# Optimization experiments

Hardware: AMD Instinct MI355X
Metric: run time of the kernel (lower is better)

The kernel has to match this reference:

```python
import jax, jax.numpy as jnp
import numpy as np

NEG_INF = -1e30  # stands in for float('-inf'); avoids nan in masked softmax edge cases


def setup_inputs() -> dict:
    key = jax.random.key(0)
    ks = jax.random.split(key, 6)
    B, N, MD, QD, AD = 64, 512, 1024, 1024, 1024
    stdv_m = 1.0 / np.sqrt(MD)
    stdv_q = 1.0 / np.sqrt(QD)
    stdv_a = 1.0 / np.sqrt(AD)
    return {
        "memory_values": jax.random.normal(ks[0], (B, N, MD), dtype=jnp.float32),
        "mask": jax.random.randint(ks[1], (B, N), 0, 2, dtype=jnp.int32),
        "query": jax.random.normal(ks[2], (B, QD), dtype=jnp.float32),
        "Wh": jax.random.uniform(ks[3], (MD, AD), jnp.float32, -stdv_m, stdv_m),
        "Ws": jax.random.uniform(ks[4], (QD, AD), jnp.float32, -stdv_q, stdv_q),
        "v": jax.random.uniform(ks[5], (AD, 1), jnp.float32, -stdv_a, stdv_a),
    }


def reference(memory_values, mask, query, Wh, Ws, v):
    # Et(i) = tanh(Hi*Wh + St*Ws) @ v ; At = softmax(Et) with masking
    tq = query @ Ws                                   # (B, AD)
    h = jnp.tanh(memory_values @ Wh + tq[:, None, :])  # (B, N, AD)
    logits = jnp.squeeze(h @ v, axis=-1)              # (B, N)

    maskf = mask.astype(logits.dtype)
    # no_cells[b] == 1 iff every cell in row b is masked out
    no_cells = jnp.prod(1.0 - maskf, axis=1, keepdims=True)  # (B, 1)
    suppress = jnp.where(maskf == 0, NEG_INF, 0.0)
    suppress = jnp.where(no_cells == 1.0, 0.0, suppress)
    weights = jax.nn.softmax(logits + suppress, axis=-1)
    weights = jnp.where(no_cells == 1.0, 0.0, weights)

    context = jnp.einsum("bn,bnd->bd", weights, memory_values)
    return context
```

## Files before the change

### kernel.cpp

```cpp
#include <hip/hip_runtime.h>
#include <cstdint>
#include <cstddef>

typedef float floatx4 __attribute__((ext_vector_type(4)));
typedef _Float16 half8_t __attribute__((ext_vector_type(8)));
typedef _Float16 half2_t __attribute__((ext_vector_type(2)));

#define AS1 __attribute__((address_space(1)))
#define AS3 __attribute__((address_space(3)))

__device__ __forceinline__ void glds16(const void* g, void* l) {
  __builtin_amdgcn_global_load_lds((const AS1 void*)g, (AS3 void*)l, 16, 0, 0);
}

__device__ __forceinline__ half2_t pkrtz(float a, float b) {
  return __builtin_bit_cast(half2_t, __builtin_amdgcn_cvt_pkrtz(a, b));
}

__device__ __forceinline__ float fast_tanh(float x) {
  float e2 = __expf(2.f * x);
  return 1.f - 2.f * __builtin_amdgcn_rcpf(e2 + 1.f);
}

__global__ __launch_bounds__(256) void k_prep(
    const float* __restrict__ mem, _Float16* __restrict__ memh,
    const float* __restrict__ Wh, _Float16* __restrict__ WhT,
    const float* __restrict__ q, const float* __restrict__ Ws,
    float* __restrict__ tq) {
  __shared__ float sh[64 * 65];
  const int bx = blockIdx.x;
  const int tid = threadIdx.x;
  if (bx >= 1280) {
    size_t i = (((size_t)(bx - 1280) << 8) + tid) << 3;
    floatx4 a = *(const floatx4*)(mem + i);
    floatx4 b = *(const floatx4*)(mem + i + 4);
    union { half2_t h2[4]; half8_t h8; } u;
    u.h2[0] = half2_t{(_Float16)a[0], (_Float16)a[1]};
    u.h2[1] = half2_t{(_Float16)a[2], (_Float16)a[3]};
    u.h2[2] = half2_t{(_Float16)b[0], (_Float16)b[1]};
    u.h2[3] = half2_t{(_Float16)b[2], (_Float16)b[3]};
    *(half8_t*)(memh + i) = u.h8;
  } else if (bx < 256) {
    int bb = bx;
    int n0 = (bb & 15) << 6, k0 = (bb >> 4) << 6;
    int tx = tid & 63, ty = tid >> 6;
    #pragma unroll
    for (int r = ty; r < 64; r += 4) sh[r * 65 + tx] = Wh[(size_t)(k0 + r) * 1024 + n0 + tx];
    __syncthreads();
    #pragma unroll
    for (int r = ty; r < 64; r += 4)
      WhT[(size_t)(n0 + r) * 1024 + k0 + tx] = (_Float16)sh[tx * 65 + r];
  } else {
    int bb = bx - 256;
    int d0 = (bb & 15) << 6, b = bb >> 4;
    int dl = tid & 63, kg = tid >> 6;
    float* qs = sh;
    float* red = sh + 1024;
    for (int k = tid; k < 1024; k += 256) qs[k] = q[(b << 10) + k];
    __syncthreads();
    float acc = 0.f;
    int kbase = kg << 8;
    #pragma unroll 8
    for (int k = 0; k < 256; ++k)
      acc += qs[kbase + k] * Ws[(size_t)(kbase + k) * 1024 + d0 + dl];
    red[(kg << 6) + dl] = acc;
    __syncthreads();
    if (kg == 0)
      tq[(b << 10) + d0 + dl] = red[dl] + red[64 + dl] + red[128 + dl] + red[192 + dl];
  }
}

__global__ void k0_transpose(const float* __restrict__ Wh, _Float16* __restrict__ WhT) {
  __shared__ float t[64][65];
  int k0 = blockIdx.y << 6, n0 = blockIdx.x << 6;
  int tx = threadIdx.x, ty = threadIdx.y;
  #pragma unroll
  for (int r = ty; r < 64; r += 4) t[r][tx] = Wh[(size_t)(k0 + r) * 1024 + n0 + tx];
  __syncthreads();
  #pragma unroll
  for (int r = ty; r < 64; r += 4)
    WhT[(size_t)(n0 + r) * 1024 + k0 + tx] = (_Float16)t[tx][r];
}

__global__ __launch_bounds__(256) void k1_tq(const float* __restrict__ q,
                                             const float* __restrict__ Ws,
                                             float* __restrict__ tq) {
  __shared__ float qs[1024];
  __shared__ float red[4][64];
  int b = blockIdx.y;
  int d0 = blockIdx.x << 6;
  int dl = threadIdx.x & 63, kg = threadIdx.x >> 6;
  for (int k = threadIdx.x; k < 1024; k += 256) qs[k] = q[(b << 10) + k];
  __syncthreads();
  float acc = 0.f;
  int kbase = kg << 8;
  #pragma unroll 8
  for (int k = 0; k < 256; ++k)
    acc += qs[kbase + k] * Ws[(size_t)(kbase + k) * 1024 + d0 + dl];
  red[kg][dl] = acc;
  __syncthreads();
  if (kg == 0)
    tq[(b << 10) + d0 + dl] = red[0][dl] + red[1][dl] + red[2][dl] + red[3][dl];
}

__global__ __launch_bounds__(512, 2) void k2_8ph(
    const _Float16* __restrict__ Ah, const _Float16* __restrict__ BT,
    const float* __restrict__ tq, const float* __restrict__ v,
    float* __restrict__ partials) {
  extern __shared__ char smem[];
  const int bid = blockIdx.x;
  const int wg = ((bid & 7) << 6) | (bid >> 3);
  const int mtile = wg >> 2, ntile = wg & 3;
  const int m0 = mtile << 8, n0 = ntile << 8;
  const int tid = threadIdx.x;
  const int w = tid >> 6, lane = tid & 63;
  const int wm = w >> 2, wn = w & 3, quad = lane >> 4, l15 = lane & 15;

  int aoff[2][4], boff[2][2];
  #pragma unroll
  for (int ks = 0; ks < 2; ++ks) {
    int swz = ((ks << 2) + quad) ^ (l15 & 7);
    #pragma unroll
    for (int i = 0; i < 4; ++i)
      aoff[ks][i] = (wm << 14) + (((i << 4) + l15) << 7) + (swz << 4);
    #pragma unroll
    for (int j = 0; j < 2; ++j)
      boff[ks][j] = 65536 + (wn << 12) + (((j << 4) + l15) << 7) + (swz << 4);
  }

  const int rr = tid >> 3, cc = tid & 7;
  const int r5 = rr & 31;
  int aSrc[2][2], bSrc[2][2], dA[2][2], dB[2][2];
  #pragma unroll
  for (int h = 0; h < 2; ++h)
    #pragma unroll
    for (int hm = 0; hm < 2; ++hm) {
      aSrc[h][hm] = ((m0 + (hm << 7) + (h << 6) + rr) << 10) + ((cc ^ (rr & 7)) << 3);
      dA[h][hm] = (((hm << 1) + h) << 13) + (w << 10);
    }
  #pragma unroll
  for (int ch = 0; ch < 2; ++ch)
    #pragma unroll
    for (int is = 0; is < 2; ++is) {
      int wnb = (is << 1) + (rr >> 5);
      bSrc[ch][is] = ((n0 + (wnb << 6) + (ch << 5) + r5) << 10) + ((cc ^ (r5 & 7)) << 3);
      dB[ch][is] = 65536 + (ch << 14) + (is << 13) + (w << 10);
    }

  floatx4 acc[8][4];
  #pragma unroll
  for (int i = 0; i < 8; ++i)
    #pragma unroll
    for (int j = 0; j < 4; ++j) acc[i][j] = floatx4{0.f, 0.f, 0.f, 0.f};

  half8_t af[2][4], bf[2][2][2];

#define STAGE_A(H, KST, OO)                                   \
  glds16(Ah + aSrc[H][0] + (KST), smem + (OO) + dA[H][0]);    \
  glds16(Ah + aSrc[H][1] + (KST), smem + (OO) + dA[H][1]);
#define STAGE_B(CH, KST, OO)                                  \
  glds16(BT + bSrc[CH][0] + (KST), smem + (OO) + dB[CH][0]);  \
  glds16(BT + bSrc[CH][1] + (KST), smem + (OO) + dB[CH][1]);
#define VMCNT8 asm volatile("s_waitcnt vmcnt(8)" ::: "memory");
#define LOAD_AF(CO, RHOFF)                                    \
  _Pragma("unroll")                                           \
  for (int ks_ = 0; ks_ < 2; ++ks_) {                         \
    _Pragma("unroll")                                         \
    for (int i_ = 0; i_ < 4; ++i_)                            \
      af[ks_][i_] = *(const half8_t*)(smem + (CO) + (RHOFF) + aoff[ks_][i_]); \
  }
#define LOAD_BF(CH, CO, CHOFF)                                \
  _Pragma("unroll")                                           \
  for (int ks_ = 0; ks_ < 2; ++ks_) {                         \
    _Pragma("unroll")                                         \
    for (int j_ = 0; j_ < 2; ++j_)                            \
      bf[CH][ks_][j_] = *(const half8_t*)(smem + (CO) + (CHOFF) + boff[ks_][j_]); \
  }
#define MFMAS(RH, CH)                                         \
  _Pragma("unroll")                                           \
  for (int ks_ = 0; ks_ < 2; ++ks_) {                         \
    _Pragma("unroll")                                         \
    for (int i_ = 0; i_ < 4; ++i_) {                          \
      _Pragma("unroll")                                       \
      for (int j_ = 0; j_ < 2; ++j_)                          \
        acc[(RH)*4 + i_][(CH)*2 + j_] = __builtin_amdgcn_mfma_f32_16x16x32_f16( \
            af[ks_][i_], bf[CH][ks_][j_], acc[(RH)*4 + i_][(CH)*2 + j_], 0, 0, 0); \
    }                                                         \
  }
#define GROUPN(CO, OO, KST)                                   \
  STAGE_A(0, KST, OO)                                         \
  STAGE_B(0, KST, OO)                                         \
  STAGE_B(1, KST, OO)                                         \
  STAGE_A(1, KST, OO)                                         \
  VMCNT8                                                      \
  __builtin_amdgcn_s_barrier();                               \
  asm volatile("" ::: "memory");                              \
  __builtin_amdgcn_s_setprio(1);                              \
  LOAD_AF(CO, 0)                                              \
  LOAD_BF(0, CO, 0)                                           \
  MFMAS(0, 0)                                                 \
  LOAD_BF(1, CO, 16384)                                       \
  MFMAS(0, 1)                                                 \
  LOAD_AF(CO, 8192)                                           \
  MFMAS(1, 0)                                                 \
  MFMAS(1, 1)                                                 \
  __builtin_amdgcn_s_setprio(0);                              \
  asm volatile("" ::: "memory");                              \
  __builtin_amdgcn_s_barrier();

  STAGE_A(0, 0, 0)
  STAGE_B(0, 0, 0)
  STAGE_B(1, 0, 0)
  STAGE_A(1, 0, 0)

  #pragma unroll 1
  for (int g2 = 0; g2 < 8; ++g2) {
    const int g = g2 << 1;
    const int kst1 = (g + 1) << 6;
    const int kst2 = (g2 == 7) ? (15 << 6) : ((g + 2) << 6);
    GROUPN(0, 32768, kst1)
    GROUPN(32768, 0, kst2)
  }

#undef GROUPN
#undef MFMAS
#undef LOAD_BF
#undef LOAD_AF
#undef VMCNT8
#undef STAGE_B
#undef STAGE_A

  asm volatile("s_waitcnt vmcnt(0)" ::: "memory");

  const int b = m0 >> 9;
  const int colb = n0 + (wn << 6) + l15;
  float tqv[4], vv[4];
  #pragma unroll
  for (int jf = 0; jf < 4; ++jf) {
    int n = colb + (jf << 4);
    tqv[jf] = tq[(b << 10) + n];
    vv[jf] = v[n];
  }
  #pragma unroll
  for (int rf = 0; rf < 8; ++rf) {
    #pragma unroll
    for (int r = 0; r < 4; ++r) {
      float s = 0.f;
      #pragma unroll
      for (int jf = 0; jf < 4; ++jf) s += fast_tanh(acc[rf][jf][r] + tqv[jf]) * vv[jf];
      s += __shfl_xor(s, 1);
      s += __shfl_xor(s, 2);
      s += __shfl_xor(s, 4);
      s += __shfl_xor(s, 8);
      if (l15 == 0) {
        int m = m0 + (wm << 7) + (rf << 4) + (quad << 2) + r;
        partials[m * 16 + (ntile << 2) + wn] = s;
      }
    }
  }
}

__global__ __launch_bounds__(256, 2) void k2_gemm_h(
    const _Float16* __restrict__ Ah, const _Float16* __restrict__ BT,
    const float* __restrict__ tq, const float* __restrict__ v,
    float* __restrict__ partials) {
  __shared__ _Float16 As[128 * 32];
  __shared__ _Float16 Bs[128 * 32];
  const int bid = blockIdx.x;
  const int mtile = ((bid >> 6) << 3) | (bid & 7);
  const int nblk = (bid >> 3) & 7;
  const int m0 = mtile << 7, n0 = nblk << 7;
  const int tid = threadIdx.x;
  const int w = tid >> 6, lane = tid & 63;
  const int wm = w >> 1, wn = w & 1, quad = lane >> 4, l15 = lane & 15;

  floatx4 acc[4][4];
  #pragma unroll
  for (int i = 0; i < 4; ++i)
    #pragma unroll
    for (int j = 0; j < 4; ++j) acc[i][j] = floatx4{0.f, 0.f, 0.f, 0.f};

  const _Float16 *gA[2], *gB[2];
  _Float16 *lA[2], *lB[2];
  #pragma unroll
  for (int t = 0; t < 2; ++t) {
    int L = (t << 8) + (w << 6) + lane;
    int row = L >> 2, jj = L & 3;
    int j = (jj - row - (row >> 2)) & 3;
    gA[t] = Ah + (size_t)(m0 + row) * 1024 + (j << 3);
    gB[t] = BT + (size_t)(n0 + row) * 1024 + (j << 3);
    lA[t] = As + (t << 11) + (w << 9);
    lB[t] = Bs + (t << 11) + (w << 9);
  }

  const half8_t *aaddr[4], *baddr[4];
  #pragma unroll
  for (int i = 0; i < 4; ++i) {
    int ar = (wm << 6) + (i << 4) + l15;
    aaddr[i] = (const half8_t*)(As + (ar << 5) + (((quad + ar + (ar >> 2)) & 3) << 3));
    int br = (wn << 6) + (i << 4) + l15;
    baddr[i] = (const half8_t*)(Bs + (br << 5) + (((quad + br + (br >> 2)) & 3) << 3));
  }

  for (int k0 = 0; k0 < 1024; k0 += 32) {
    __syncthreads();
    glds16(gA[0] + k0, lA[0]);
    glds16(gA[1] + k0, lA[1]);
    glds16(gB[0] + k0, lB[0]);
    glds16(gB[1] + k0, lB[1]);
    __syncthreads();
    half8_t af[4], bfr[4];
    #pragma unroll
    for (int i = 0; i < 4; ++i) af[i] = *aaddr[i];
    #pragma unroll
    for (int j = 0; j < 4; ++j) bfr[j] = *baddr[j];
    #pragma unroll
    for (int i = 0; i < 4; ++i)
      #pragma unroll
      for (int j = 0; j < 4; ++j)
        acc[i][j] = __builtin_amdgcn_mfma_f32_16x16x32_f16(af[i], bfr[j], acc[i][j], 0, 0, 0);
  }

  const int b = m0 >> 9;
  const int colbase = n0 + (wn << 6) + l15;
  float tqv[4], vv[4];
  #pragma unroll
  for (int j = 0; j < 4; ++j) {
    int n = colbase + (j << 4);
    tqv[j] = tq[(b << 10) + n];
    vv[j] = v[n];
  }
  #pragma unroll
  for (int i = 0; i < 4; ++i) {
    #pragma unroll
    for (int r = 0; r < 4; ++r) {
      float s = 0.f;
      #pragma unroll
      for (int j = 0; j < 4; ++j) s += fast_tanh(acc[i][j][r] + tqv[j]) * vv[j];
      s += __shfl_xor(s, 1);
      s += __shfl_xor(s, 2);
      s += __shfl_xor(s, 4);
      s += __shfl_xor(s, 8);
      if (l15 == 0) {
        int m = m0 + (wm << 6) + (i << 4) + (quad << 2) + r;
        partials[m * 16 + (nblk << 1) + wn] = s;
      }
    }
  }
}

__global__ __launch_bounds__(256, 2) void k2_gemm_f32(
    const float* __restrict__ A, const _Float16* __restrict__ BT,
    const float* __restrict__ tq, const float* __restrict__ v,
    float* __restrict__ partials) {
  __shared__ float As[128 * 32];
  __shared__ _Float16 Bs[128 * 32];
  const int bid = blockIdx.x;
  const int mtile = ((bid >> 6) << 3) | (bid & 7);
  const int nblk = (bid >> 3) & 7;
  const int m0 = mtile << 7, n0 = nblk << 7;
  const int tid = threadIdx.x;
  const int w = tid >> 6, lane = tid & 63;
  const int wm = w >> 1, wn = w & 1, quad = lane >> 4, l15 = lane & 15;

  floatx4 acc[4][4];
  #pragma unroll
  for (int i = 0; i < 4; ++i)
    #pragma unroll
    for (int j = 0; j < 4; ++j) acc[i][j] = floatx4{0.f, 0.f, 0.f, 0.f};

  const float* gA[4];
  float* lA[4];
  #pragma unroll
  for (int t = 0; t < 4; ++t) {
    int L = (t << 8) + (w << 6) + lane;
    int row = L >> 3, jj = L & 7;
    int j = (jj - row) & 7;
    gA[t] = A + (size_t)(m0 + row) * 1024 + (j << 2);
    lA[t] = As + (t << 10) + (w << 8);
  }
  const _Float16* gB[2];
  _Float16* lB[2];
  #pragma unroll
  for (int t = 0; t < 2; ++t) {
    int L = (t << 8) + (w << 6) + lane;
    int row = L >> 2, jj = L & 3;
    int j = (jj - row - (row >> 2)) & 3;
    gB[t] = BT + (size_t)(n0 + row) * 1024 + (j << 3);
    lB[t] = Bs + (t << 11) + (w << 9);
  }
  const floatx4* aaddr[4][2];
  #pragma unroll
  for (int i = 0; i < 4; ++i) {
    int row = (wm << 6) + (i << 4) + l15;
    #pragma unroll
    for (int h = 0; h < 2; ++h) {
      int pos = ((quad << 1) + h + row) & 7;
      aaddr[i][h] = (const floatx4*)(As + (row << 5) + (pos << 2));
    }
  }
  const half8_t* baddr[4];
  #pragma unroll
  for (int j = 0; j < 4; ++j) {
    int row = (wn << 6) + (j << 4) + l15;
    int pos = (quad + row + (row >> 2)) & 3;
    baddr[j] = (const half8_t*)(Bs + (row << 5) + (pos << 3));
  }
  for (int k0 = 0; k0 < 1024; k0 += 32) {
    __syncthreads();
    glds16(gA[0] + k0, lA[0]);
    glds16(gA[1] + k0, lA[1]);
    glds16(gA[2] + k0, lA[2]);
    glds16(gA[3] + k0, lA[3]);
    glds16(gB[0] + k0, lB[0]);
    glds16(gB[1] + k0, lB[1]);
    __syncthreads();
    half8_t af[4], bfr[4];
    #pragma unroll
    for (int i = 0; i < 4; ++i) {
      floatx4 x = *aaddr[i][0], y = *aaddr[i][1];
      union { half2_t h2[4]; half8_t h8; } u;
      u.h2[0] = pkrtz(x[0], x[1]);
      u.h2[1] = pkrtz(x[2], x[3]);
      u.h2[2] = pkrtz(y[0], y[1]);
      u.h2[3] = pkrtz(y[2], y[3]);
      af[i] = u.h8;
    }
    #pragma unroll
    for (int j = 0; j < 4; ++j) bfr[j] = *baddr[j];
    #pragma unroll
    for (int i = 0; i < 4; ++i)
      #pragma unroll
      for (int j = 0; j < 4; ++j)
        acc[i][j] = __builtin_amdgcn_mfma_f32_16x16x32_f16(af[i], bfr[j], acc[i][j], 0, 0, 0);
  }
  const int b = m0 >> 9;
  const int colbase = n0 + (wn << 6) + l15;
  float tqv[4], vv[4];
  #pragma unroll
  for (int j = 0; j < 4; ++j) {
    int n = colbase + (j << 4);
    tqv[j] = tq[(b << 10) + n];
    vv[j] = v[n];
  }
  #pragma unroll
  for (int i = 0; i < 4; ++i) {
    #pragma unroll
    for (int r = 0; r < 4; ++r) {
      float s = 0.f;
      #pragma unroll
      for (int j = 0; j < 4; ++j) s += fast_tanh(acc[i][j][r] + tqv[j]) * vv[j];
      s += __shfl_xor(s, 1);
      s += __shfl_xor(s, 2);
      s += __shfl_xor(s, 4);
      s += __shfl_xor(s, 8);
      if (l15 == 0) {
        int m = m0 + (wm << 6) + (i << 4) + (quad << 2) + r;
        partials[m * 16 + (nblk << 1) + wn] = s;
      }
    }
  }
}

__global__ __launch_bounds__(512) void k3_softmax(const float* __restrict__ partials,
                                                  const int* __restrict__ mask,
                                                  float* __restrict__ weights) {
  int b = blockIdx.x;
  int n = threadIdx.x;
  int m = (b << 9) + n;
  float s = 0.f;
  #pragma unroll
  for (int i = 0; i < 16; ++i) s += partials[m * 16 + i];
  int mk = mask[m];
  float logit = mk ? s : -1e30f;
  __shared__ float red[8];
  float x = logit;
  #pragma unroll
  for (int off = 32; off > 0; off >>= 1) x = fmaxf(x, __shfl_xor(x, off));
  if ((n & 63) == 0) red[n >> 6] = x;
  __syncthreads();
  float mx = red[0];
  #pragma unroll
  for (int i = 1; i < 8; ++i) mx = fmaxf(mx, red[i]);
  float e = mk ? __expf(logit - mx) : 0.f;
  float ss = e;
  #pragma unroll
  for (int off = 32; off > 0; off >>= 1) ss += __shfl_xor(ss, off);
  __syncthreads();
  if ((n & 63) == 0) red[n >> 6] = ss;
  __syncthreads();
  float tot = 0.f;
  #pragma unroll
  for (int i = 0; i < 8; ++i) tot += red[i];
  weights[m] = (tot > 0.f) ? e / tot : 0.f;
}

__global__ void k4_ctx_h(const _Float16* __restrict__ memh,
                         const float* __restrict__ weights, float* __restrict__ ctxp) {
  int nc = blockIdx.x, b = blockIdx.y;
  int d = threadIdx.x << 3;
  float acc[8] = {0.f, 0.f, 0.f, 0.f, 0.f, 0.f, 0.f, 0.f};
  int nbase = nc << 5;
  for (int n = nbase; n < nbase + 32; ++n) {
    float wv = weights[(b << 9) + n];
    half8_t x = *(const half8_t*)(memh + ((size_t)((b << 9) + n) << 10) + d);
    #pragma unroll
    for (int k = 0; k < 8; ++k) acc[k] += wv * (float)x[k];
  }
  float* o = ctxp + ((size_t)((b << 4) + nc) << 10) + d;
  #pragma unroll
  for (int k = 0; k < 8; ++k) o[k] = acc[k];
}

__global__ void k5_reduce16(const float* __restrict__ ctxp, float* __restrict__ out) {
  int i = (blockIdx.x << 8) + threadIdx.x;
  int b = i >> 10, d = i & 1023;
  float s = 0.f;
  #pragma unroll
  for (int cc = 0; cc < 16; ++cc) s += ctxp[((size_t)((b << 4) + cc) << 10) + d];
  out[i] = s;
}

__global__ void k4_ctx_f32(const float* __restrict__ mem, const float* __restrict__ weights,
                           float* __restrict__ ctxp) {
  int nc = blockIdx.x, b = blockIdx.y;
  int d = threadIdx.x << 3;
  floatx4 a0 = {0.f, 0.f, 0.f, 0.f}, a1 = {0.f, 0.f, 0.f, 0.f};
  int nbase = nc << 6;
  for (int n = nbase; n < nbase + 64; ++n) {
    float wv = weights[(b << 9) + n];
    const floatx4* p = (const floatx4*)(mem + ((size_t)((b << 9) + n) << 10) + d);
    a0 += wv * p[0];
    a1 += wv * p[1];
  }
  floatx4* o = (floatx4*)(ctxp + ((size_t)((b << 3) + nc) << 10) + d);
  o[0] = a0;
  o[1] = a1;
}

__global__ void k5_reduce8(const float* __restrict__ ctxp, float* __restrict__ out) {
  int i = (blockIdx.x << 8) + threadIdx.x;
  int b = i >> 10, d = i & 1023;
  float s = 0.f;
  #pragma unroll
  for (int cc = 0; cc < 8; ++cc) s += ctxp[((size_t)((b << 3) + cc) << 10) + d];
  out[i] = s;
}

extern "C" void kernel_launch(void* const* d_in, const int* in_sizes, int n_in,
                              void* d_out, int out_size, void* d_ws, size_t ws_size,
                              hipStream_t stream) {
  const float* mem = (const float*)d_in[0];
  const int* mask = (const int*)d_in[1];
  const float* query = (const float*)d_in[2];
  const float* Wh = (const float*)d_in[3];
  const float* Ws = (const float*)d_in[4];
  const float* v = (const float*)d_in[5];
  float* out = (float*)d_out;

  char* ws = (char*)d_ws;
  const size_t need16 = (73ull << 20);

  if (ws_size >= need16) {
    _Float16* memh = (_Float16*)ws;
    _Float16* WhT = (_Float16*)(ws + (64ull << 20));
    float* partials = (float*)(ws + (66ull << 20));
    float* tq = (float*)(ws + (68ull << 20));
    float* weights = (float*)(ws + (68ull << 20) + (256 << 10));
    float* ctxp = (float*)(ws + (69ull << 20));

    static int use8 = -1;
    if (use8 < 0) {
      use8 = (hipFuncSetAttribute((const void*)k2_8ph,
                                  hipFuncAttributeMaxDynamicSharedMemorySize,
                                  131072) == hipSuccess) ? 1 : 0;
    }

    k_prep<<<17664, 256, 0, stream>>>(mem, memh, Wh, WhT, query, Ws, tq);
    if (use8)
      k2_8ph<<<512, 512, 131072, stream>>>(memh, WhT, tq, v, partials);
    else
      k2_gemm_h<<<2048, 256, 0, stream>>>(memh, WhT, tq, v, partials);
    k3_softmax<<<64, 512, 0, stream>>>(partials, mask, weights);
    k4_ctx_h<<<dim3(16, 64), 128, 0, stream>>>(memh, weights, ctxp);
    k5_reduce16<<<256, 256, 0, stream>>>(ctxp, out);
  } else {
    _Float16* WhT = (_Float16*)ws;
    float* partials = (float*)(ws + ((size_t)2 << 20));
    float* tq = (float*)(ws + ((size_t)4 << 20));
    float* weights = (float*)(ws + ((size_t)4 << 20) + (256 << 10));
    float* ctxp = (float*)(ws + ((size_t)9 << 19));

    k0_transpose<<<dim3(16, 16), dim3(64, 4), 0, stream>>>(Wh, WhT);
    k1_tq<<<dim3(16, 64), 256, 0, stream>>>(query, Ws, tq);
    k2_gemm_f32<<<2048, 256, 0, stream>>>(mem, WhT, tq, v, partials);
    k3_softmax<<<64, 512, 0, stream>>>(partials, mask, weights);
    k4_ctx_f32<<<dim3(8, 64), 128, 0, stream>>>(mem, weights, ctxp);
    k5_reduce8<<<256, 256, 0, stream>>>(ctxp, out);
  }
}
```

Measured before the change: 301.1 us.

## Interleave global-to-LDS staging with MFMA quadrants using finer barriers

Restructures the GEMM main loop so that each K-group is split into four MFMA quadrants. Each quadrant is bracketed by barriers and finer vmcnt waits, and the staging of the next tile's A/B chunks is spread between them instead of being issued all at once before a single barrier. The intent is to overlap global-to-LDS loads with MFMA work more evenly and reduce stalls on one large wait. The cost is more barriers per iteration, and the correctness of the chosen vmcnt counts matters.

```diff
diff --git a/kernel.cpp b/kernel.cpp
--- a/kernel.cpp
+++ b/kernel.cpp
@@ -161,7 +161,8 @@
 #define STAGE_B(CH, KST, OO)                                  \
   glds16(BT + bSrc[CH][0] + (KST), smem + (OO) + dB[CH][0]);  \
   glds16(BT + bSrc[CH][1] + (KST), smem + (OO) + dB[CH][1]);
-#define VMCNT8 asm volatile("s_waitcnt vmcnt(8)" ::: "memory");
+#define VM(N) asm volatile("s_waitcnt vmcnt(" #N ")" ::: "memory");
+#define BAR __builtin_amdgcn_s_barrier();
 #define LOAD_AF(CO, RHOFF)                                    \
   _Pragma("unroll")                                           \
   for (int ks_ = 0; ks_ < 2; ++ks_) {                         \
@@ -187,46 +188,62 @@
             af[ks_][i_], bf[CH][ks_][j_], acc[(RH)*4 + i_][(CH)*2 + j_], 0, 0, 0); \
     }                                                         \
   }
-#define GROUPN(CO, OO, KST)                                   \
+#define PRIO_MFMA(RH, CH)                                     \
+  __builtin_amdgcn_s_setprio(1);                              \
+  MFMAS(RH, CH)                                               \
+  __builtin_amdgcn_s_setprio(0);
+#define GROUPT(CO, OO, KST)                                   \
+                                              \
+  LOAD_AF(CO, 0)                                              \
+  LOAD_BF(0, CO, 0)                                           \
+  VM(2)                                                       \
   STAGE_A(0, KST, OO)                                         \
   STAGE_B(0, KST, OO)                                         \
+  BAR                                                         \
+  PRIO_MFMA(0, 0)                                             \
+  BAR                                                         \
+                                              \
+  LOAD_BF(1, CO, 16384)                                       \
+  VM(4)                                                       \
   STAGE_B(1, KST, OO)                                         \
+  BAR                                                         \
+  PRIO_MFMA(0, 1)                                             \
+  BAR                                                         \
+                                              \
+  LOAD_AF(CO, 8192)                                           \
   STAGE_A(1, KST, OO)                                         \
-  VMCNT8                                                      \
-  __builtin_amdgcn_s_barrier();                               \
-  asm volatile("" ::: "memory");                              \
-  __builtin_amdgcn_s_setprio(1);                              \
-  LOAD_AF(CO, 0)                                              \
-  LOAD_BF(0, CO, 0)                                           \
-  MFMAS(0, 0)                                                 \
-  LOAD_BF(1, CO, 16384)                                       \
-  MFMAS(0, 1)                                                 \
-  LOAD_AF(CO, 8192)                                           \
-  MFMAS(1, 0)                                                 \
-  MFMAS(1, 1)                                                 \
-  __builtin_amdgcn_s_setprio(0);                              \
-  asm volatile("" ::: "memory");                              \
-  __builtin_amdgcn_s_barrier();
+  BAR                                                         \
+  PRIO_MFMA(1, 0)                                             \
+  BAR                                                         \
+                                              \
+  VM(4)                                                       \
+  BAR                                                         \
+  PRIO_MFMA(1, 1)                                             \
+  BAR
 
   STAGE_A(0, 0, 0)
   STAGE_B(0, 0, 0)
   STAGE_B(1, 0, 0)
   STAGE_A(1, 0, 0)
+  VM(4)
+  BAR
 
   #pragma unroll 1
   for (int g2 = 0; g2 < 8; ++g2) {
     const int g = g2 << 1;
     const int kst1 = (g + 1) << 6;
     const int kst2 = (g2 == 7) ? (15 << 6) : ((g + 2) << 6);
-    GROUPN(0, 32768, kst1)
-    GROUPN(32768, 0, kst2)
-  }
-
-#undef GROUPN
+    GROUPT(0, 32768, kst1)
+    GROUPT(32768, 0, kst2)
+  }
+
+#undef GROUPT
+#undef PRIO_MFMA
 #undef MFMAS
 #undef LOAD_BF
 #undef LOAD_AF
-#undef VMCNT8
+#undef BAR
+#undef VM
 #undef STAGE_B
 #undef STAGE_A
 
```

Measured after the change: 295.1 us. -2.0%, faster.
